# Optimization experiments

Measured on AMD Instinct MI355X. Metric: run time of the kernel, lower is better.

The kernel has to match this reference:

```python
import jax, jax.numpy as jnp
import numpy as np

KERNEL = 3  # 2*half_size + 1 with half_size=1
ITER = 20


def _pool(v):
    # MaxPool2d(kernel=3, stride=1, padding=1) == SAME max reduce_window on NCHW
    return jax.lax.reduce_window(v, -jnp.inf, jax.lax.max,
                                 (1, 1, KERNEL, KERNEL), (1, 1, 1, 1), 'SAME')


def _erode(v):
    return -_pool(-v)


def setup_inputs() -> dict:
    key = jax.random.key(0)
    x = jax.random.normal(key, (16, 1, 1024, 1024), dtype=jnp.float32)
    return {"x": x}


def reference(x):
    skel0 = x - _pool(_erode(x))  # open(x) = dilate(erode(x))

    def step(carry, _):
        xc, skel = carry
        xc = _erode(xc)
        skel = skel + (xc - _pool(_erode(xc)))
        return (xc, skel), None

    (_, skel), _ = jax.lax.scan(step, (x, skel0), None, length=ITER)
    return skel
```

## Files before the change

kernel.cpp:

```cpp
#include <hip/hip_runtime.h>


static constexpr int W = 1024, H = 1024, NIMG = 16;
static constexpr int RCH = 64;
static constexpr int WPB = 4;
static constexpr float BIG = 3.0e38f;

__device__ __forceinline__ float min3f(float a, float b, float c) { return fminf(fminf(a, b), c); }
__device__ __forceinline__ float max3f(float a, float b, float c) { return fmaxf(fmaxf(a, b), c); }

__device__ __forceinline__ float dpp_left(float v) {
    return __int_as_float(__builtin_amdgcn_mov_dpp(__float_as_int(v), 0x138, 0xF, 0xF, true));
}
__device__ __forceinline__ float dpp_right(float v) {
    return __int_as_float(__builtin_amdgcn_mov_dpp(__float_as_int(v), 0x130, 0xF, 0xF, true));
}

template<bool FIRST, bool WRITE_E, bool EDGE, bool LE, bool RE, int MODE>
__device__ __forceinline__
void pipe_step2(int t, int y0, int gx,
                bool leftEdge, bool rightEdge, bool lane_ok,
                const float* __restrict__ in, float* __restrict__ eo,
                float* __restrict__ sk,
                float4 (&OB)[7], float4 (&MB)[7], float4& OD, float4& MD,
                float4 (&acc)[8], float4 (&pf)[2])
{
    float4 cur0, cur1;
    if (!EDGE || (unsigned)t < (unsigned)H)       cur0 = pf[0];
    else                                          cur0 = make_float4(BIG, BIG, BIG, BIG);
    if (!EDGE || (unsigned)(t + 1) < (unsigned)H) cur1 = pf[1];
    else                                          cur1 = make_float4(BIG, BIG, BIG, BIG);
    {
        const int n0 = t + 2, n1 = t + 3;
        if (MODE != 1 || ((!EDGE || (unsigned)n0 < (unsigned)H) && n0 <= y0 + RCH + 7))
            pf[0] = *(const float4*)&in[(size_t)n0 * W + gx];
        if (MODE != 1 || ((!EDGE || (unsigned)n1 < (unsigned)H) && n1 <= y0 + RCH + 7))
            pf[1] = *(const float4*)&in[(size_t)n1 * W + gx];
    }

#pragma unroll
    for (int s = 0; s < 7; ++s) {
        const float4 fOld = OB[s];
        const float4 fMid = MB[s];

        float4 vm0, vm1;
        vm0.x = min3f(fOld.x, fMid.x, cur0.x);
        vm0.y = min3f(fOld.y, fMid.y, cur0.y);
        vm0.z = min3f(fOld.z, fMid.z, cur0.z);
        vm0.w = min3f(fOld.w, fMid.w, cur0.w);
        vm1.x = min3f(fMid.x, cur0.x, cur1.x);
        vm1.y = min3f(fMid.y, cur0.y, cur1.y);
        vm1.z = min3f(fMid.z, cur0.z, cur1.z);
        vm1.w = min3f(fMid.w, cur0.w, cur1.w);
        float l0 = dpp_left(vm0.w), r0 = dpp_right(vm0.x);
        float l1 = dpp_left(vm1.w), r1 = dpp_right(vm1.x);
        if (LE && leftEdge)  { l0 = BIG; l1 = BIG; }
        if (RE && rightEdge) { r0 = BIG; r1 = BIG; }
        float4 en0, en1;
        en0.x = min3f(l0,    vm0.x, vm0.y);
        en0.y = min3f(vm0.x, vm0.y, vm0.z);
        en0.z = min3f(vm0.y, vm0.z, vm0.w);
        en0.w = min3f(vm0.z, vm0.w, r0);
        en1.x = min3f(l1,    vm1.x, vm1.y);
        en1.y = min3f(vm1.x, vm1.y, vm1.z);
        en1.z = min3f(vm1.y, vm1.z, vm1.w);
        en1.w = min3f(vm1.z, vm1.w, r1);

        if (MODE != 0) {
            float4 gOld, gMid;
            if (s < 6) { gOld = OB[s + 1]; gMid = MB[s + 1]; }
            else       { gOld = OD;        gMid = MD;        }
            float4 vx0, vx1;
            if (!EDGE) {
                vx0.x = max3f(gOld.x, gMid.x, en0.x);
                vx0.y = max3f(gOld.y, gMid.y, en0.y);
                vx0.z = max3f(gOld.z, gMid.z, en0.z);
                vx0.w = max3f(gOld.w, gMid.w, en0.w);
                vx1.x = max3f(gMid.x, en0.x, en1.x);
                vx1.y = max3f(gMid.y, en0.y, en1.y);
                vx1.z = max3f(gMid.z, en0.z, en1.z);
                vx1.w = max3f(gMid.w, en0.w, en1.w);
            } else {
                const bool topOK0 = (t - s - 3) >= 0, botOK0 = (t - s - 1) < H;
                const bool topOK1 = (t - s - 2) >= 0, botOK1 = (t - s) < H;
                vx0.x = max3f(topOK0 ? gOld.x : -BIG, gMid.x, botOK0 ? en0.x : -BIG);
                vx0.y = max3f(topOK0 ? gOld.y : -BIG, gMid.y, botOK0 ? en0.y : -BIG);
                vx0.z = max3f(topOK0 ? gOld.z : -BIG, gMid.z, botOK0 ? en0.z : -BIG);
                vx0.w = max3f(topOK0 ? gOld.w : -BIG, gMid.w, botOK0 ? en0.w : -BIG);
                vx1.x = max3f(topOK1 ? gMid.x : -BIG, en0.x, botOK1 ? en1.x : -BIG);
                vx1.y = max3f(topOK1 ? gMid.y : -BIG, en0.y, botOK1 ? en1.y : -BIG);
                vx1.z = max3f(topOK1 ? gMid.z : -BIG, en0.z, botOK1 ? en1.z : -BIG);
                vx1.w = max3f(topOK1 ? gMid.w : -BIG, en0.w, botOK1 ? en1.w : -BIG);
            }
            float dl0 = dpp_left(vx0.w), dr0 = dpp_right(vx0.x);
            float dl1 = dpp_left(vx1.w), dr1 = dpp_right(vx1.x);
            if (LE && leftEdge)  { dl0 = -BIG; dl1 = -BIG; }
            if (RE && rightEdge) { dr0 = -BIG; dr1 = -BIG; }
            float4 dn0, dn1;
            dn0.x = max3f(dl0,   vx0.x, vx0.y);
            dn0.y = max3f(vx0.x, vx0.y, vx0.z);
            dn0.z = max3f(vx0.y, vx0.z, vx0.w);
            dn0.w = max3f(vx0.z, vx0.w, dr0);
            dn1.x = max3f(dl1,   vx1.x, vx1.y);
            dn1.y = max3f(vx1.x, vx1.y, vx1.z);
            dn1.z = max3f(vx1.y, vx1.z, vx1.w);
            dn1.w = max3f(vx1.z, vx1.w, dr1);

            if (FIRST && s == 0) {
                acc[6].x = fOld.x - dn0.x;  acc[6].y = fOld.y - dn0.y;
                acc[6].z = fOld.z - dn0.z;  acc[6].w = fOld.w - dn0.w;
                acc[7].x = fMid.x - dn1.x;  acc[7].y = fMid.y - dn1.y;
                acc[7].z = fMid.z - dn1.z;  acc[7].w = fMid.w - dn1.w;
            } else {
                acc[6 - s].x += fOld.x - dn0.x;  acc[6 - s].y += fOld.y - dn0.y;
                acc[6 - s].z += fOld.z - dn0.z;  acc[6 - s].w += fOld.w - dn0.w;
                acc[7 - s].x += fMid.x - dn1.x;  acc[7 - s].y += fMid.y - dn1.y;
                acc[7 - s].z += fMid.z - dn1.z;  acc[7 - s].w += fMid.w - dn1.w;
            }
        }

        OB[s] = cur0;
        MB[s] = cur1;

        if (s == 6) {
            if (WRITE_E && MODE != 0) {
                const int er0 = t - 7, er1 = t - 6;
                if (MODE == 2) {
                    if (lane_ok) {
                        *(float4*)&eo[(size_t)er0 * W + gx] = en0;
                        *(float4*)&eo[(size_t)er1 * W + gx] = en1;
                    }
                } else {
                    if (er0 >= y0 && er0 < y0 + RCH && lane_ok)
                        *(float4*)&eo[(size_t)er0 * W + gx] = en0;
                    if (er1 >= y0 && er1 < y0 + RCH && lane_ok)
                        *(float4*)&eo[(size_t)er1 * W + gx] = en1;
                }
            }
            OD = en0;
            MD = en1;
        }
        cur0 = en0;
        cur1 = en1;
    }

    if (MODE != 0) {
        if (MODE == 2) {
            if (lane_ok) {
                *(float4*)&sk[(size_t)(t - 8) * W + gx] = acc[0];
                *(float4*)&sk[(size_t)(t - 7) * W + gx] = acc[1];
            }
        } else {
            if (t >= y0 + 8 && lane_ok) {
                *(float4*)&sk[(size_t)(t - 8) * W + gx] = acc[0];
                *(float4*)&sk[(size_t)(t - 7) * W + gx] = acc[1];
            }
        }
#pragma unroll
        for (int j = 0; j < 6; ++j) acc[j] = acc[j + 2];
        if (!FIRST) {
            if (MODE == 2) {
                acc[6] = *(const float4*)&sk[(size_t)t * W + gx];
                acc[7] = *(const float4*)&sk[(size_t)(t + 1) * W + gx];
            } else {
                if (t >= y0 && t < y0 + RCH)
                    acc[6] = *(const float4*)&sk[(size_t)t * W + gx];
                if (t + 1 >= y0 && t + 1 < y0 + RCH)
                    acc[7] = *(const float4*)&sk[(size_t)(t + 1) * W + gx];
            }
        }
    }
}

template<bool FIRST, bool WRITE_E, bool LE, bool RE>
__device__ __forceinline__
void sweep_int(int y0, int gx, bool leftEdge, bool rightEdge, bool lane_ok,
               const float* __restrict__ in, float* __restrict__ eo,
               float* __restrict__ sk)
{
    float4 OB[7], MB[7], OD, MD, acc[8], pf[2];
    const float4 big4 = make_float4(BIG, BIG, BIG, BIG);
    const float4 z4   = make_float4(0.f, 0.f, 0.f, 0.f);
#pragma unroll
    for (int s = 0; s < 7; ++s) { OB[s] = big4; MB[s] = big4; }
    OD = big4; MD = big4;
#pragma unroll
    for (int j = 0; j < 8; ++j) acc[j] = z4;
    pf[0] = *(const float4*)&in[(size_t)(y0 - 8) * W + gx];
    pf[1] = *(const float4*)&in[(size_t)(y0 - 7) * W + gx];

    int t = y0 - 8;
#pragma unroll
    for (int i = 0; i < 4; ++i, t += 2)
        pipe_step2<FIRST, WRITE_E, false, LE, RE, 0>(t, y0, gx, leftEdge, rightEdge, lane_ok,
                                                     in, eo, sk, OB, MB, OD, MD, acc, pf);
#pragma unroll 1
    for (int i = 0; i < 4; ++i, t += 2)
        pipe_step2<FIRST, WRITE_E, false, LE, RE, 1>(t, y0, gx, leftEdge, rightEdge, lane_ok,
                                                     in, eo, sk, OB, MB, OD, MD, acc, pf);
#pragma unroll 1
    for (int i = 0; i < 28; ++i, t += 2)
        pipe_step2<FIRST, WRITE_E, false, LE, RE, 2>(t, y0, gx, leftEdge, rightEdge, lane_ok,
                                                     in, eo, sk, OB, MB, OD, MD, acc, pf);
#pragma unroll 1
    for (int i = 0; i < 4; ++i, t += 2)
        pipe_step2<FIRST, WRITE_E, false, LE, RE, 1>(t, y0, gx, leftEdge, rightEdge, lane_ok,
                                                     in, eo, sk, OB, MB, OD, MD, acc, pf);
}

template<bool FIRST, bool WRITE_E, bool LE, bool RE>
__device__ __forceinline__
void sweep_edge(int y0, int gx, bool leftEdge, bool rightEdge, bool lane_ok,
                const float* __restrict__ in, float* __restrict__ eo,
                float* __restrict__ sk)
{
    float4 OB[7], MB[7], OD, MD, acc[8], pf[2];
    const float4 big4 = make_float4(BIG, BIG, BIG, BIG);
    const float4 z4   = make_float4(0.f, 0.f, 0.f, 0.f);
#pragma unroll
    for (int s = 0; s < 7; ++s) { OB[s] = big4; MB[s] = big4; }
    OD = big4; MD = big4;
#pragma unroll
    for (int j = 0; j < 8; ++j) acc[j] = z4;
    pf[0] = big4; pf[1] = big4;
    {
        const int r0 = y0 - 8, r1 = y0 - 7;
        if (r0 >= 0) pf[0] = *(const float4*)&in[(size_t)r0 * W + gx];
        if (r1 >= 0) pf[1] = *(const float4*)&in[(size_t)r1 * W + gx];
    }

    int t = y0 - 8;
#pragma unroll 1
    for (int i = 0; i < (RCH + 16) / 2; ++i, t += 2)
        pipe_step2<FIRST, WRITE_E, true, LE, RE, 1>(t, y0, gx, leftEdge, rightEdge, lane_ok,
                                                    in, eo, sk, OB, MB, OD, MD, acc, pf);
}

template<bool FIRST, bool WRITE_E>
__global__ __launch_bounds__(WPB * 64)
void skel_pipe(const float* __restrict__ ein, float* __restrict__ eout,
               float* __restrict__ skel)
{
    const int lane = threadIdx.x;
    const int bx = blockIdx.x;
    const int y0 = (blockIdx.y * WPB + (int)threadIdx.y) * RCH;
    const int img = blockIdx.z;
    const int x0 = (bx == 4) ? 768 : bx * 240;
    const int gx = x0 + 4 * lane;

    const size_t base = (size_t)img * (size_t)(W * H);
    const float* __restrict__ in = ein + base;
    float* __restrict__ eo = eout + base;
    float* __restrict__ sk = skel + base;

    const bool leftEdge  = (gx == 0);
    const bool rightEdge = (gx + 4 == W);
    const int own_lo = (bx == 0) ? 0 : ((bx == 4) ? 968 : x0 + 8);
    const int own_hi = (bx == 4) ? W : x0 + 248;
    const bool lane_ok = (gx >= own_lo) && (gx < own_hi);

    const bool interior = (y0 >= 32 && y0 <= H - RCH - 32);

    if (bx == 0) {
        if (interior) sweep_int <FIRST, WRITE_E, true,  false>(y0, gx, leftEdge, rightEdge, lane_ok, in, eo, sk);
        else          sweep_edge<FIRST, WRITE_E, true,  false>(y0, gx, leftEdge, rightEdge, lane_ok, in, eo, sk);
    } else if (bx == 4) {
        if (interior) sweep_int <FIRST, WRITE_E, false, true >(y0, gx, leftEdge, rightEdge, lane_ok, in, eo, sk);
        else          sweep_edge<FIRST, WRITE_E, false, true >(y0, gx, leftEdge, rightEdge, lane_ok, in, eo, sk);
    } else {
        if (interior) sweep_int <FIRST, WRITE_E, false, false>(y0, gx, leftEdge, rightEdge, lane_ok, in, eo, sk);
        else          sweep_edge<FIRST, WRITE_E, false, false>(y0, gx, leftEdge, rightEdge, lane_ok, in, eo, sk);
    }
}

extern "C" void kernel_launch(void* const* d_in, const int* in_sizes, int n_in,
                              void* d_out, int out_size, void* d_ws, size_t ws_size,
                              hipStream_t stream)
{
    const float* x = (const float*)d_in[0];
    float* skel = (float*)d_out;
    const size_t n = (size_t)NIMG * W * H;

    float* e0 = (float*)d_ws;
    float* e1 = e0 + n;

    dim3 grid(5, H / (RCH * WPB), NIMG);
    dim3 block(64, WPB);

    skel_pipe<true,  true ><<<grid, block, 0, stream>>>(x,  e0, skel);
    skel_pipe<false, true ><<<grid, block, 0, stream>>>(e0, e1, skel);
    skel_pipe<false, false><<<grid, block, 0, stream>>>(e1, e0, skel);
}
```

Baseline: 359.0 us.

## Narrow per-lane tile to float2 columns and shrink row chunks to raise parallelism

```diff
diff --git a/kernel.cpp b/kernel.cpp
--- a/kernel.cpp
+++ b/kernel.cpp
@@ -2,8 +2,9 @@
 
 
 static constexpr int W = 1024, H = 1024, NIMG = 16;
-static constexpr int RCH = 64;
-static constexpr int WPB = 4;
+static constexpr int RCH = 32;
+static constexpr int WPB = 2;
+static constexpr int NBAND = 9;
 static constexpr float BIG = 3.0e38f;
 
 __device__ __forceinline__ float min3f(float a, float b, float c) { return fminf(fminf(a, b), c); }
@@ -22,100 +23,76 @@
                 bool leftEdge, bool rightEdge, bool lane_ok,
                 const float* __restrict__ in, float* __restrict__ eo,
                 float* __restrict__ sk,
-                float4 (&OB)[7], float4 (&MB)[7], float4& OD, float4& MD,
-                float4 (&acc)[8], float4 (&pf)[2])
-{
-    float4 cur0, cur1;
+                float2 (&OB)[7], float2 (&MB)[7], float2& OD, float2& MD,
+                float2 (&acc)[8], float2 (&pf)[2])
+{
+    float2 cur0, cur1;
     if (!EDGE || (unsigned)t < (unsigned)H)       cur0 = pf[0];
-    else                                          cur0 = make_float4(BIG, BIG, BIG, BIG);
+    else                                          cur0 = make_float2(BIG, BIG);
     if (!EDGE || (unsigned)(t + 1) < (unsigned)H) cur1 = pf[1];
-    else                                          cur1 = make_float4(BIG, BIG, BIG, BIG);
+    else                                          cur1 = make_float2(BIG, BIG);
     {
         const int n0 = t + 2, n1 = t + 3;
         if (MODE != 1 || ((!EDGE || (unsigned)n0 < (unsigned)H) && n0 <= y0 + RCH + 7))
-            pf[0] = *(const float4*)&in[(size_t)n0 * W + gx];
+            pf[0] = *(const float2*)&in[(size_t)n0 * W + gx];
         if (MODE != 1 || ((!EDGE || (unsigned)n1 < (unsigned)H) && n1 <= y0 + RCH + 7))
-            pf[1] = *(const float4*)&in[(size_t)n1 * W + gx];
+            pf[1] = *(const float2*)&in[(size_t)n1 * W + gx];
     }
 
 #pragma unroll
     for (int s = 0; s < 7; ++s) {
-        const float4 fOld = OB[s];
-        const float4 fMid = MB[s];
-
-        float4 vm0, vm1;
+        const float2 fOld = OB[s];
+        const float2 fMid = MB[s];
+
+        float2 vm0, vm1;
         vm0.x = min3f(fOld.x, fMid.x, cur0.x);
         vm0.y = min3f(fOld.y, fMid.y, cur0.y);
-        vm0.z = min3f(fOld.z, fMid.z, cur0.z);
-        vm0.w = min3f(fOld.w, fMid.w, cur0.w);
         vm1.x = min3f(fMid.x, cur0.x, cur1.x);
         vm1.y = min3f(fMid.y, cur0.y, cur1.y);
-        vm1.z = min3f(fMid.z, cur0.z, cur1.z);
-        vm1.w = min3f(fMid.w, cur0.w, cur1.w);
-        float l0 = dpp_left(vm0.w), r0 = dpp_right(vm0.x);
-        float l1 = dpp_left(vm1.w), r1 = dpp_right(vm1.x);
+        float l0 = dpp_left(vm0.y), r0 = dpp_right(vm0.x);
+        float l1 = dpp_left(vm1.y), r1 = dpp_right(vm1.x);
         if (LE && leftEdge)  { l0 = BIG; l1 = BIG; }
         if (RE && rightEdge) { r0 = BIG; r1 = BIG; }
-        float4 en0, en1;
+        float2 en0, en1;
         en0.x = min3f(l0,    vm0.x, vm0.y);
-        en0.y = min3f(vm0.x, vm0.y, vm0.z);
-        en0.z = min3f(vm0.y, vm0.z, vm0.w);
-        en0.w = min3f(vm0.z, vm0.w, r0);
+        en0.y = min3f(vm0.x, vm0.y, r0);
         en1.x = min3f(l1,    vm1.x, vm1.y);
-        en1.y = min3f(vm1.x, vm1.y, vm1.z);
-        en1.z = min3f(vm1.y, vm1.z, vm1.w);
-        en1.w = min3f(vm1.z, vm1.w, r1);
+        en1.y = min3f(vm1.x, vm1.y, r1);
 
         if (MODE != 0) {
-            float4 gOld, gMid;
+            float2 gOld, gMid;
             if (s < 6) { gOld = OB[s + 1]; gMid = MB[s + 1]; }
             else       { gOld = OD;        gMid = MD;        }
-            float4 vx0, vx1;
+            float2 vx0, vx1;
             if (!EDGE) {
                 vx0.x = max3f(gOld.x, gMid.x, en0.x);
                 vx0.y = max3f(gOld.y, gMid.y, en0.y);
-                vx0.z = max3f(gOld.z, gMid.z, en0.z);
-                vx0.w = max3f(gOld.w, gMid.w, en0.w);
                 vx1.x = max3f(gMid.x, en0.x, en1.x);
                 vx1.y = max3f(gMid.y, en0.y, en1.y);
-                vx1.z = max3f(gMid.z, en0.z, en1.z);
-                vx1.w = max3f(gMid.w, en0.w, en1.w);
             } else {
                 const bool topOK0 = (t - s - 3) >= 0, botOK0 = (t - s - 1) < H;
                 const bool topOK1 = (t - s - 2) >= 0, botOK1 = (t - s) < H;
                 vx0.x = max3f(topOK0 ? gOld.x : -BIG, gMid.x, botOK0 ? en0.x : -BIG);
                 vx0.y = max3f(topOK0 ? gOld.y : -BIG, gMid.y, botOK0 ? en0.y : -BIG);
-                vx0.z = max3f(topOK0 ? gOld.z : -BIG, gMid.z, botOK0 ? en0.z : -BIG);
-                vx0.w = max3f(topOK0 ? gOld.w : -BIG, gMid.w, botOK0 ? en0.w : -BIG);
                 vx1.x = max3f(topOK1 ? gMid.x : -BIG, en0.x, botOK1 ? en1.x : -BIG);
                 vx1.y = max3f(topOK1 ? gMid.y : -BIG, en0.y, botOK1 ? en1.y : -BIG);
-                vx1.z = max3f(topOK1 ? gMid.z : -BIG, en0.z, botOK1 ? en1.z : -BIG);
-                vx1.w = max3f(topOK1 ? gMid.w : -BIG, en0.w, botOK1 ? en1.w : -BIG);
-            }
-            float dl0 = dpp_left(vx0.w), dr0 = dpp_right(vx0.x);
-            float dl1 = dpp_left(vx1.w), dr1 = dpp_right(vx1.x);
+            }
+            float dl0 = dpp_left(vx0.y), dr0 = dpp_right(vx0.x);
+            float dl1 = dpp_left(vx1.y), dr1 = dpp_right(vx1.x);
             if (LE && leftEdge)  { dl0 = -BIG; dl1 = -BIG; }
             if (RE && rightEdge) { dr0 = -BIG; dr1 = -BIG; }
-            float4 dn0, dn1;
+            float2 dn0, dn1;
             dn0.x = max3f(dl0,   vx0.x, vx0.y);
-            dn0.y = max3f(vx0.x, vx0.y, vx0.z);
-            dn0.z = max3f(vx0.y, vx0.z, vx0.w);
-            dn0.w = max3f(vx0.z, vx0.w, dr0);
+            dn0.y = max3f(vx0.x, vx0.y, dr0);
             dn1.x = max3f(dl1,   vx1.x, vx1.y);
-            dn1.y = max3f(vx1.x, vx1.y, vx1.z);
-            dn1.z = max3f(vx1.y, vx1.z, vx1.w);
-            dn1.w = max3f(vx1.z, vx1.w, dr1);
+            dn1.y = max3f(vx1.x, vx1.y, dr1);
 
             if (FIRST && s == 0) {
                 acc[6].x = fOld.x - dn0.x;  acc[6].y = fOld.y - dn0.y;
-                acc[6].z = fOld.z - dn0.z;  acc[6].w = fOld.w - dn0.w;
                 acc[7].x = fMid.x - dn1.x;  acc[7].y = fMid.y - dn1.y;
-                acc[7].z = fMid.z - dn1.z;  acc[7].w = fMid.w - dn1.w;
             } else {
                 acc[6 - s].x += fOld.x - dn0.x;  acc[6 - s].y += fOld.y - dn0.y;
-                acc[6 - s].z += fOld.z - dn0.z;  acc[6 - s].w += fOld.w - dn0.w;
                 acc[7 - s].x += fMid.x - dn1.x;  acc[7 - s].y += fMid.y - dn1.y;
-                acc[7 - s].z += fMid.z - dn1.z;  acc[7 - s].w += fMid.w - dn1.w;
             }
         }
 
@@ -127,14 +104,14 @@
                 const int er0 = t - 7, er1 = t - 6;
                 if (MODE == 2) {
                     if (lane_ok) {
-                        *(float4*)&eo[(size_t)er0 * W + gx] = en0;
-                        *(float4*)&eo[(size_t)er1 * W + gx] = en1;
+                        *(float2*)&eo[(size_t)er0 * W + gx] = en0;
+                        *(float2*)&eo[(size_t)er1 * W + gx] = en1;
                     }
                 } else {
                     if (er0 >= y0 && er0 < y0 + RCH && lane_ok)
-                        *(float4*)&eo[(size_t)er0 * W + gx] = en0;
+                        *(float2*)&eo[(size_t)er0 * W + gx] = en0;
                     if (er1 >= y0 && er1 < y0 + RCH && lane_ok)
-                        *(float4*)&eo[(size_t)er1 * W + gx] = en1;
+                        *(float2*)&eo[(size_t)er1 * W + gx] = en1;
                 }
             }
             OD = en0;
@@ -147,26 +124,26 @@
     if (MODE != 0) {
         if (MODE == 2) {
             if (lane_ok) {
-                *(float4*)&sk[(size_t)(t - 8) * W + gx] = acc[0];
-                *(float4*)&sk[(size_t)(t - 7) * W + gx] = acc[1];
+                *(float2*)&sk[(size_t)(t - 8) * W + gx] = acc[0];
+                *(float2*)&sk[(size_t)(t - 7) * W + gx] = acc[1];
             }
         } else {
             if (t >= y0 + 8 && lane_ok) {
-                *(float4*)&sk[(size_t)(t - 8) * W + gx] = acc[0];
-                *(float4*)&sk[(size_t)(t - 7) * W + gx] = acc[1];
+                *(float2*)&sk[(size_t)(t - 8) * W + gx] = acc[0];
+                *(float2*)&sk[(size_t)(t - 7) * W + gx] = acc[1];
             }
         }
 #pragma unroll
         for (int j = 0; j < 6; ++j) acc[j] = acc[j + 2];
         if (!FIRST) {
             if (MODE == 2) {
-                acc[6] = *(const float4*)&sk[(size_t)t * W + gx];
-                acc[7] = *(const float4*)&sk[(size_t)(t + 1) * W + gx];
+                acc[6] = *(const float2*)&sk[(size_t)t * W + gx];
+                acc[7] = *(const float2*)&sk[(size_t)(t + 1) * W + gx];
             } else {
                 if (t >= y0 && t < y0 + RCH)
-                    acc[6] = *(const float4*)&sk[(size_t)t * W + gx];
+                    acc[6] = *(const float2*)&sk[(size_t)t * W + gx];
                 if (t + 1 >= y0 && t + 1 < y0 + RCH)
-                    acc[7] = *(const float4*)&sk[(size_t)(t + 1) * W + gx];
+                    acc[7] = *(const float2*)&sk[(size_t)(t + 1) * W + gx];
             }
         }
     }
@@ -178,16 +155,16 @@
                const float* __restrict__ in, float* __restrict__ eo,
                float* __restrict__ sk)
 {
-    float4 OB[7], MB[7], OD, MD, acc[8], pf[2];
-    const float4 big4 = make_float4(BIG, BIG, BIG, BIG);
-    const float4 z4   = make_float4(0.f, 0.f, 0.f, 0.f);
-#pragma unroll
-    for (int s = 0; s < 7; ++s) { OB[s] = big4; MB[s] = big4; }
-    OD = big4; MD = big4;
-#pragma unroll
-    for (int j = 0; j < 8; ++j) acc[j] = z4;
-    pf[0] = *(const float4*)&in[(size_t)(y0 - 8) * W + gx];
-    pf[1] = *(const float4*)&in[(size_t)(y0 - 7) * W + gx];
+    float2 OB[7], MB[7], OD, MD, acc[8], pf[2];
+    const float2 big2 = make_float2(BIG, BIG);
+    const float2 z2   = make_float2(0.f, 0.f);
+#pragma unroll
+    for (int s = 0; s < 7; ++s) { OB[s] = big2; MB[s] = big2; }
+    OD = big2; MD = big2;
+#pragma unroll
+    for (int j = 0; j < 8; ++j) acc[j] = z2;
+    pf[0] = *(const float2*)&in[(size_t)(y0 - 8) * W + gx];
+    pf[1] = *(const float2*)&in[(size_t)(y0 - 7) * W + gx];
 
     int t = y0 - 8;
 #pragma unroll
@@ -199,7 +176,7 @@
         pipe_step2<FIRST, WRITE_E, false, LE, RE, 1>(t, y0, gx, leftEdge, rightEdge, lane_ok,
                                                      in, eo, sk, OB, MB, OD, MD, acc, pf);
 #pragma unroll 1
-    for (int i = 0; i < 28; ++i, t += 2)
+    for (int i = 0; i < 12; ++i, t += 2)
         pipe_step2<FIRST, WRITE_E, false, LE, RE, 2>(t, y0, gx, leftEdge, rightEdge, lane_ok,
                                                      in, eo, sk, OB, MB, OD, MD, acc, pf);
 #pragma unroll 1
@@ -214,19 +191,19 @@
                 const float* __restrict__ in, float* __restrict__ eo,
                 float* __restrict__ sk)
 {
-    float4 OB[7], MB[7], OD, MD, acc[8], pf[2];
-    const float4 big4 = make_float4(BIG, BIG, BIG, BIG);
-    const float4 z4   = make_float4(0.f, 0.f, 0.f, 0.f);
-#pragma unroll
-    for (int s = 0; s < 7; ++s) { OB[s] = big4; MB[s] = big4; }
-    OD = big4; MD = big4;
-#pragma unroll
-    for (int j = 0; j < 8; ++j) acc[j] = z4;
-    pf[0] = big4; pf[1] = big4;
+    float2 OB[7], MB[7], OD, MD, acc[8], pf[2];
+    const float2 big2 = make_float2(BIG, BIG);
+    const float2 z2   = make_float2(0.f, 0.f);
+#pragma unroll
+    for (int s = 0; s < 7; ++s) { OB[s] = big2; MB[s] = big2; }
+    OD = big2; MD = big2;
+#pragma unroll
+    for (int j = 0; j < 8; ++j) acc[j] = z2;
+    pf[0] = big2; pf[1] = big2;
     {
         const int r0 = y0 - 8, r1 = y0 - 7;
-        if (r0 >= 0) pf[0] = *(const float4*)&in[(size_t)r0 * W + gx];
-        if (r1 >= 0) pf[1] = *(const float4*)&in[(size_t)r1 * W + gx];
+        if (r0 >= 0) pf[0] = *(const float2*)&in[(size_t)r0 * W + gx];
+        if (r1 >= 0) pf[1] = *(const float2*)&in[(size_t)r1 * W + gx];
     }
 
     int t = y0 - 8;
@@ -245,8 +222,8 @@
     const int bx = blockIdx.x;
     const int y0 = (blockIdx.y * WPB + (int)threadIdx.y) * RCH;
     const int img = blockIdx.z;
-    const int x0 = (bx == 4) ? 768 : bx * 240;
-    const int gx = x0 + 4 * lane;
+    const int x0 = (bx == 0) ? 0 : ((bx == NBAND - 1) ? (W - 128) : 112 * bx);
+    const int gx = x0 + 2 * lane;
 
     const size_t base = (size_t)img * (size_t)(W * H);
     const float* __restrict__ in = ein + base;
@@ -254,9 +231,9 @@
     float* __restrict__ sk = skel + base;
 
     const bool leftEdge  = (gx == 0);
-    const bool rightEdge = (gx + 4 == W);
-    const int own_lo = (bx == 0) ? 0 : ((bx == 4) ? 968 : x0 + 8);
-    const int own_hi = (bx == 4) ? W : x0 + 248;
+    const bool rightEdge = (gx + 2 == W);
+    const int own_lo = (bx == 0) ? 0 : 112 * bx + 8;
+    const int own_hi = (bx == NBAND - 1) ? W : 112 * (bx + 1) + 8;
     const bool lane_ok = (gx >= own_lo) && (gx < own_hi);
 
     const bool interior = (y0 >= 32 && y0 <= H - RCH - 32);
@@ -264,7 +241,7 @@
     if (bx == 0) {
         if (interior) sweep_int <FIRST, WRITE_E, true,  false>(y0, gx, leftEdge, rightEdge, lane_ok, in, eo, sk);
         else          sweep_edge<FIRST, WRITE_E, true,  false>(y0, gx, leftEdge, rightEdge, lane_ok, in, eo, sk);
-    } else if (bx == 4) {
+    } else if (bx == NBAND - 1) {
         if (interior) sweep_int <FIRST, WRITE_E, false, true >(y0, gx, leftEdge, rightEdge, lane_ok, in, eo, sk);
         else          sweep_edge<FIRST, WRITE_E, false, true >(y0, gx, leftEdge, rightEdge, lane_ok, in, eo, sk);
     } else {
@@ -284,7 +261,7 @@
     float* e0 = (float*)d_ws;
     float* e1 = e0 + n;
 
-    dim3 grid(5, H / (RCH * WPB), NIMG);
+    dim3 grid(NBAND, H / (RCH * WPB), NIMG);
     dim3 block(64, WPB);
 
     skel_pipe<true,  true ><<<grid, block, 0, stream>>>(x,  e0, skel);
```

Measured after the change: 302.9 us. 1.19x faster.
